# Optimization experiments

Hardware: AMD Instinct MI355X
Metric: run time of the kernel (lower is better)

Reference implementation:

```python
import jax, jax.numpy as jnp
import numpy as np

# ---- Cl(4,1) Cayley table (signature [1,1,1,1,-1]), basis blades indexed by 5-bit mask ----
_METRIC = np.array([1, 1, 1, 1, -1], dtype=np.float32)

def _build_gp_map():
    T = np.zeros((32, 32, 32), dtype=np.float32)
    for a in range(32):
        for b in range(32):
            # canonical reordering sign (count generator swaps)
            s, aa = 0, a >> 1
            while aa:
                s += bin(aa & b).count('1')
                aa >>= 1
            sign = -1.0 if (s & 1) else 1.0
            # metric contribution of annihilated common generators
            common = a & b
            for i in range(5):
                if (common >> i) & 1:
                    sign *= _METRIC[i]
            T[a, b, a ^ b] = sign  # e_a * e_b = sign * e_{a XOR b}
    return T

GP_MAP = _build_gp_map()  # [32, 32, 32], one signed nonzero per (a,b) pair

IN_FEATURES = 256
OUT_FEATURES = 256
BATCH, SEQ = 4, 512


def setup_inputs() -> dict:
    key = jax.random.key(0)
    kx, kw = jax.random.split(key)
    x = jax.random.normal(kx, (BATCH, SEQ, IN_FEATURES, 32), dtype=jnp.float32)
    # Versor init: std = sqrt(2 / (fan_in * 32))
    std = (2.0 / (IN_FEATURES * 32)) ** 0.5
    weight = jax.random.normal(kw, (OUT_FEATURES, IN_FEATURES, 32), dtype=jnp.float32) * std
    return {"x": x, "weight": weight}


def normalize_cl41(out, eps=1e-6):
    # Normalize each output multivector by its Euclidean norm over the 32 basis coeffs.
    norm = jnp.sqrt(jnp.sum(out * out, axis=-1, keepdims=True) + eps)
    return out / norm


def reference(x, weight):
    gp = jnp.asarray(GP_MAP, dtype=x.dtype)  # [j, l, k]
    # W_op[o,i,l,k] = sum_j weight[o,i,j] * gp[j,l,k]
    W_op = jnp.einsum('oij,jlk->oilk', weight, gp)
    # out[b,s,o,k] = sum_{i,l} x[b,s,i,l] * W_op[o,i,l,k]
    out = jnp.einsum('bsil,oilk->bsok', x, W_op)
    return normalize_cl41(out)
```

## Files before the change

kernel.cpp:

```cpp
#include <hip/hip_runtime.h>
#include <stdint.h>

#define AS1 __attribute__((address_space(1)))
#define AS3 __attribute__((address_space(3)))

typedef __attribute__((ext_vector_type(8))) short bf16x8;
typedef __attribute__((ext_vector_type(4))) float f32x4;

struct Mono { int col[4]; int ph[4]; };

constexpr Mono mono_mul(Mono A, Mono B) {
    Mono R{};
    for (int r = 0; r < 4; ++r) {
        int k = A.col[r];
        R.col[r] = B.col[k];
        R.ph[r] = (A.ph[r] + B.ph[k]) & 3;
    }
    return R;
}

constexpr Mono gen(int g) {
    Mono E{};
    for (int r = 0; r < 4; ++r) {
        int r1 = (r >> 1) & 1, r0 = r & 1;
        if (g == 0)      { E.col[r] = r ^ 2; E.ph[r] = 0; }
        else if (g == 1) { E.col[r] = r ^ 2; E.ph[r] = r1 ? 1 : 3; }
        else if (g == 2) { E.col[r] = r ^ 1; E.ph[r] = r1 ? 2 : 0; }
        else if (g == 3) { E.col[r] = r ^ 1; E.ph[r] = ((r1 ? 2 : 0) + (r0 ? 1 : 3)) & 3; }
        else             { E.col[r] = r;     E.ph[r] = (1 + (r1 ? 2 : 0) + (r0 ? 2 : 0)) & 3; }
    }
    return E;
}

struct Blades { Mono m[32]; };
constexpr Blades make_blades() {
    Blades B{};
    for (int A = 0; A < 32; ++A) {
        Mono M{};
        for (int r = 0; r < 4; ++r) { M.col[r] = r; M.ph[r] = 0; }
        for (int g = 0; g < 5; ++g)
            if ((A >> g) & 1) M = mono_mul(M, gen(g));
        B.m[A] = M;
    }
    return B;
}
constexpr Blades BL = make_blades();

struct FwdTab { int bl[4][4][2][4]; float sg[4][4][2][4]; };
constexpr FwdTab make_fwd() {
    FwdTab T{};
    int cnt[4][4][2] = {};
    for (int A = 0; A < 32; ++A)
        for (int r = 0; r < 4; ++r) {
            int c = BL.m[A].col[r], p = BL.m[A].ph[r];
            int rc = p & 1;
            int& n = cnt[r][c][rc];
            T.bl[r][c][rc][n] = A;
            T.sg[r][c][rc][n] = (p & 2) ? -1.f : 1.f;
            ++n;
        }
    return T;
}
constexpr FwdTab FT = make_fwd();

__device__ inline unsigned short f2bf(float f) {
    uint32_t u = __float_as_uint(f);
    u += 0x7FFFu + ((u >> 16) & 1u);
    return (unsigned short)(u >> 16);
}

__global__ __launch_bounds__(256) void xform_kernel(const float* __restrict__ x,
                                                    const float* __restrict__ w,
                                                    unsigned short* __restrict__ Xb,
                                                    unsigned short* __restrict__ Wr) {
    __shared__ alignas(16) float XS[8192];
    if (blockIdx.x < 2048) {
        int tid = threadIdx.x;
        const float4* xp = (const float4*)(x + (size_t)blockIdx.x * 8192);
        float4 ld[8];
#pragma unroll
        for (int r = 0; r < 8; ++r) ld[r] = xp[r * 256 + tid];
#pragma unroll
        for (int r = 0; r < 8; ++r) {
            int U = r * 256 + tid;
            int L = (U & ~7) | ((U & 7) ^ ((U >> 3) & 7));
            *(float4*)&XS[L * 4] = ld[r];
        }
        __syncthreads();
        float v[32];
#pragma unroll
        for (int q = 0; q < 8; ++q) {
            int L = tid * 8 + (q ^ (tid & 7));
            float4 f = *(const float4*)&XS[L * 4];
            v[q * 4 + 0] = f.x; v[q * 4 + 1] = f.y; v[q * 4 + 2] = f.z; v[q * 4 + 3] = f.w;
        }
        int t = blockIdx.x * 256 + tid;
        int i = t & 255, n = t >> 8;
#pragma unroll
        for (int b = 0; b < 4; ++b) {
            union { unsigned short s[8]; uint4 u; } r;
#pragma unroll
            for (int c = 0; c < 4; ++c)
#pragma unroll
                for (int rc = 0; rc < 2; ++rc) {
                    float s = 0.f;
#pragma unroll
                    for (int j = 0; j < 4; ++j)
                        s += FT.sg[c][b][rc][j] * v[FT.bl[c][b][rc][j]];
                    r.s[c * 2 + rc] = f2bf(s);
                }
            *((uint4*)(Xb + (size_t)(n * 4 + b) * 2048 + i * 8)) = r.u;
        }
    } else {
        int t = (blockIdx.x - 2048) * 256 + threadIdx.x;
        int i = t & 255, o = t >> 8;
        float v[32];
        const float4* wp = (const float4*)(w + (size_t)t * 32);
#pragma unroll
        for (int q = 0; q < 8; ++q) {
            float4 f = wp[q];
            v[q * 4 + 0] = f.x; v[q * 4 + 1] = f.y; v[q * 4 + 2] = f.z; v[q * 4 + 3] = f.w;
        }
        float Re[4][4], Im[4][4];
#pragma unroll
        for (int a = 0; a < 4; ++a)
#pragma unroll
            for (int c = 0; c < 4; ++c) {
                float sr = 0.f, si = 0.f;
#pragma unroll
                for (int j = 0; j < 4; ++j) {
                    sr += FT.sg[a][c][0][j] * v[FT.bl[a][c][0][j]];
                    si += FT.sg[a][c][1][j] * v[FT.bl[a][c][1][j]];
                }
                Re[a][c] = sr; Im[a][c] = si;
            }
#pragma unroll
        for (int ra = 0; ra < 2; ++ra)
#pragma unroll
            for (int a = 0; a < 4; ++a) {
                int m = o * 8 + ra * 4 + a;
                union { unsigned short s[8]; uint4 u; } r;
#pragma unroll
                for (int c = 0; c < 4; ++c) {
                    float v0 = ra == 0 ? Re[a][c] : Im[a][c];
                    float v1 = ra == 0 ? -Im[a][c] : Re[a][c];
                    r.s[c * 2 + 0] = f2bf(v0);
                    r.s[c * 2 + 1] = f2bf(v1);
                }
                *((uint4*)(Wr + (size_t)m * 2048 + i * 8)) = r.u;
            }
    }
}

__global__ __launch_bounds__(512, 2) void gemm_kernel(const unsigned short* __restrict__ A,
                                                      const unsigned short* __restrict__ B,
                                                      float* __restrict__ out) {
    const int K = 2048;
    const int NT = 64;
    __shared__ alignas(16) unsigned short SM[4 * 16384];

    const int tid = threadIdx.x;
    const int wid = tid >> 6, lane = tid & 63;
    const int lm = lane & 15, quad = lane >> 4;
    const int wm = wid >> 2, wn = wid & 3;
    const int row0 = blockIdx.y * 256;
    const int col0 = blockIdx.x * 256;

    size_t gA[2], gB[2];
    int ldsA[2], ldsB[2];
#pragma unroll
    for (int p = 0; p < 2; ++p) {
        int g = p * 512 + tid;
        int r = g >> 2, c = g & 3;
        int sc = c ^ ((r >> 1) & 3);
        gA[p] = (size_t)(row0 + r) * K + sc * 8;
        gB[p] = (size_t)(col0 + r) * K + sc * 8;
        ldsA[p] = (p * 512 + wid * 64) * 8;
        ldsB[p] = 8192 + (p * 512 + wid * 64) * 8;
    }

    const int swz = (lm >> 1) & 3;
    const int aoff = (wm * 128 + lm) * 32 + (quad ^ swz) * 8;
    const int boff = 8192 + (wn * 64 + lm) * 32 + (quad ^ swz) * 8;

    f32x4 acc[8][4];
#pragma unroll
    for (int i = 0; i < 8; ++i)
#pragma unroll
        for (int j = 0; j < 4; ++j) acc[i][j] = (f32x4){0.f, 0.f, 0.f, 0.f};

    auto ISSUE = [&](int t) {
        const int bb = (t & 3) * 16384;
        const int k0 = t * 32;
#pragma unroll
        for (int p = 0; p < 2; ++p) {
            __builtin_amdgcn_global_load_lds((const AS1 void*)(A + gA[p] + k0),
                                             (AS3 void*)(&SM[bb + ldsA[p]]), 16, 0, 0);
            __builtin_amdgcn_global_load_lds((const AS1 void*)(B + gB[p] + k0),
                                             (AS3 void*)(&SM[bb + ldsB[p]]), 16, 0, 0);
        }
    };
    auto COMPUTE = [&](int t) {
        const int bb = (t & 3) * 16384;
        bf16x8 av[8], bv[4];
#pragma unroll
        for (int fn = 0; fn < 4; ++fn) bv[fn] = *(const bf16x8*)&SM[bb + boff + fn * 512];
#pragma unroll
        for (int fm = 0; fm < 8; ++fm) av[fm] = *(const bf16x8*)&SM[bb + aoff + fm * 512];
        __builtin_amdgcn_s_setprio(1);
#pragma unroll
        for (int fm = 0; fm < 8; ++fm)
#pragma unroll
            for (int fn = 0; fn < 4; ++fn)
                acc[fm][fn] = __builtin_amdgcn_mfma_f32_16x16x32_bf16(av[fm], bv[fn],
                                                                      acc[fm][fn], 0, 0, 0);
        __builtin_amdgcn_s_setprio(0);
    };

    ISSUE(0); ISSUE(1); ISSUE(2);
    for (int t = 0; t < NT - 3; ++t) {
        asm volatile("s_waitcnt vmcnt(8)" ::: "memory");
        __builtin_amdgcn_s_barrier();
        ISSUE(t + 3);
        COMPUTE(t);
    }
    asm volatile("s_waitcnt vmcnt(8)" ::: "memory");
    __builtin_amdgcn_s_barrier();
    COMPUTE(NT - 3);
    asm volatile("s_waitcnt vmcnt(4)" ::: "memory");
    __builtin_amdgcn_s_barrier();
    COMPUTE(NT - 2);
    asm volatile("s_waitcnt vmcnt(0)" ::: "memory");
    __builtin_amdgcn_s_barrier();
    COMPUTE(NT - 1);
    __syncthreads();

    float* scrw = (float*)SM + wid * 2048;
    const int nl = lane >> 2, ol = lane & 3;
#pragma unroll
    for (int s = 0; s < 4; ++s) {
#pragma unroll
        for (int h = 0; h < 2; ++h)
#pragma unroll
            for (int fn = 0; fn < 4; ++fn)
#pragma unroll
                for (int r = 0; r < 4; ++r) {
                    int rw = h * 16 + quad * 4 + r;
                    int cc = (fn * 16 + lm) ^ (quad << 3);
                    scrw[rw * 64 + cc] = acc[s * 2 + h][fn][r];
                }
        asm volatile("s_waitcnt lgkmcnt(0)" ::: "memory");
        float V[32];
#pragma unroll
        for (int u = 0; u < 8; ++u) {
            int row = ol * 8 + u;
            int cb = (nl * 4) ^ (((row >> 2) & 3) << 3);
            float4 f = *(const float4*)&scrw[row * 64 + cb];
            int vi = (u >> 2) * 16 + (u & 3) * 4;
            V[vi + 0] = f.x; V[vi + 1] = f.y; V[vi + 2] = f.z; V[vi + 3] = f.w;
        }
        float xa[32];
        float ss = 0.f;
#pragma unroll
        for (int Ab = 0; Ab < 32; ++Ab) {
            float sv = 0.f;
#pragma unroll
            for (int a = 0; a < 4; ++a) {
                const int c = BL.m[Ab].col[a];
                const int p = BL.m[Ab].ph[a];
                float vv = V[(p & 1) * 16 + a * 4 + c];
                sv += (p & 2) ? -vv : vv;
            }
            sv *= 0.25f;
            xa[Ab] = sv;
            ss += sv * sv;
        }
        float inv = rsqrtf(ss + 1e-6f);
        int o = (row0 >> 3) + wm * 16 + s * 4 + ol;
        int n = (col0 >> 2) + wn * 16 + nl;
        float4* op = (float4*)(out + ((size_t)n * 256 + o) * 32);
#pragma unroll
        for (int q = 0; q < 8; ++q) {
            float4 f;
            f.x = xa[q * 4 + 0] * inv; f.y = xa[q * 4 + 1] * inv;
            f.z = xa[q * 4 + 2] * inv; f.w = xa[q * 4 + 3] * inv;
            op[q] = f;
        }
        asm volatile("s_waitcnt lgkmcnt(0)" ::: "memory");
    }
}

extern "C" void kernel_launch(void* const* d_in, const int* in_sizes, int n_in,
                              void* d_out, int out_size, void* d_ws, size_t ws_size,
                              hipStream_t stream) {
    const float* x = (const float*)d_in[0];
    const float* w = (const float*)d_in[1];
    float* out = (float*)d_out;

    unsigned short* Wr = (unsigned short*)d_ws;
    unsigned short* Xb = (unsigned short*)((char*)d_ws + 8388608);

    hipLaunchKernelGGL(xform_kernel, dim3(2304),  dim3(256), 0, stream, x, w, Xb, Wr);
    hipLaunchKernelGGL(gemm_kernel,  dim3(32, 8), dim3(512), 0, stream, Wr, Xb, out);
}
```

Measured before the change: 193.9 us.

## Split each K-step into two MFMA halves interleaved with A/B prefetch

The main GEMM loop is folded into a single loop with per-iteration wait counts. Each K-tile is processed in two halves: load half of the A fragments, issue the A prefetch for tile t+3, run 16 MFMAs, then barrier, load the other A half, issue the B prefetch, and run the remaining MFMAs. The goal is to spread global-to-LDS traffic across the compute phase and to hold fewer A fragment registers at once. The cost is an extra barrier per half-step and conditional code inside the loop, which may limit unrolling and scheduling.

```diff
diff --git a/kernel.cpp b/kernel.cpp
--- a/kernel.cpp
+++ b/kernel.cpp
@@ -189,50 +189,59 @@
 #pragma unroll
         for (int j = 0; j < 4; ++j) acc[i][j] = (f32x4){0.f, 0.f, 0.f, 0.f};
 
-    auto ISSUE = [&](int t) {
+    auto ISSUE_A = [&](int t) {
         const int bb = (t & 3) * 16384;
         const int k0 = t * 32;
 #pragma unroll
-        for (int p = 0; p < 2; ++p) {
+        for (int p = 0; p < 2; ++p)
             __builtin_amdgcn_global_load_lds((const AS1 void*)(A + gA[p] + k0),
                                              (AS3 void*)(&SM[bb + ldsA[p]]), 16, 0, 0);
+    };
+    auto ISSUE_B = [&](int t) {
+        const int bb = (t & 3) * 16384;
+        const int k0 = t * 32;
+#pragma unroll
+        for (int p = 0; p < 2; ++p)
             __builtin_amdgcn_global_load_lds((const AS1 void*)(B + gB[p] + k0),
                                              (AS3 void*)(&SM[bb + ldsB[p]]), 16, 0, 0);
-        }
     };
-    auto COMPUTE = [&](int t) {
+
+    ISSUE_A(0); ISSUE_B(0); ISSUE_A(1); ISSUE_B(1); ISSUE_A(2); ISSUE_B(2);
+
+    for (int t = 0; t < NT; ++t) {
         const int bb = (t & 3) * 16384;
-        bf16x8 av[8], bv[4];
+        if (t <= NT - 3)      asm volatile("s_waitcnt vmcnt(8)" ::: "memory");
+        else if (t == NT - 2) asm volatile("s_waitcnt vmcnt(4)" ::: "memory");
+        else                  asm volatile("s_waitcnt vmcnt(0)" ::: "memory");
+        __builtin_amdgcn_s_barrier();
+        bf16x8 a0[4], a1[4], bv[4];
 #pragma unroll
         for (int fn = 0; fn < 4; ++fn) bv[fn] = *(const bf16x8*)&SM[bb + boff + fn * 512];
 #pragma unroll
-        for (int fm = 0; fm < 8; ++fm) av[fm] = *(const bf16x8*)&SM[bb + aoff + fm * 512];
+        for (int f = 0; f < 4; ++f) a0[f] = *(const bf16x8*)&SM[bb + aoff + f * 512];
+        if (t < NT - 3) ISSUE_A(t + 3);
         __builtin_amdgcn_s_setprio(1);
 #pragma unroll
-        for (int fm = 0; fm < 8; ++fm)
-#pragma unroll
-            for (int fn = 0; fn < 4; ++fn)
-                acc[fm][fn] = __builtin_amdgcn_mfma_f32_16x16x32_bf16(av[fm], bv[fn],
-                                                                      acc[fm][fn], 0, 0, 0);
+        for (int f = 0; f < 4; ++f)
+#pragma unroll
+            for (int n = 0; n < 4; ++n)
+                acc[f][n] = __builtin_amdgcn_mfma_f32_16x16x32_bf16(a0[f], bv[n],
+                                                                    acc[f][n], 0, 0, 0);
         __builtin_amdgcn_s_setprio(0);
-    };
-
-    ISSUE(0); ISSUE(1); ISSUE(2);
-    for (int t = 0; t < NT - 3; ++t) {
-        asm volatile("s_waitcnt vmcnt(8)" ::: "memory");
         __builtin_amdgcn_s_barrier();
-        ISSUE(t + 3);
-        COMPUTE(t);
-    }
-    asm volatile("s_waitcnt vmcnt(8)" ::: "memory");
-    __builtin_amdgcn_s_barrier();
-    COMPUTE(NT - 3);
-    asm volatile("s_waitcnt vmcnt(4)" ::: "memory");
-    __builtin_amdgcn_s_barrier();
-    COMPUTE(NT - 2);
-    asm volatile("s_waitcnt vmcnt(0)" ::: "memory");
-    __builtin_amdgcn_s_barrier();
-    COMPUTE(NT - 1);
+#pragma unroll
+        for (int f = 0; f < 4; ++f) a1[f] = *(const bf16x8*)&SM[bb + aoff + (f + 4) * 512];
+        if (t < NT - 3) ISSUE_B(t + 3);
+        __builtin_amdgcn_s_setprio(1);
+#pragma unroll
+        for (int f = 0; f < 4; ++f)
+#pragma unroll
+            for (int n = 0; n < 4; ++n)
+                acc[f + 4][n] = __builtin_amdgcn_mfma_f32_16x16x32_bf16(a1[f], bv[n],
+                                                                        acc[f + 4][n], 0, 0, 0);
+        __builtin_amdgcn_s_setprio(0);
+        __builtin_amdgcn_s_barrier();
+    }
     __syncthreads();
 
     float* scrw = (float*)SM + wid * 2048;
```

Measured after the change: 194.8 us. Within noise of the previous version (+0.5%).
